# Kernel optimization log

Hardware: AMD Instinct MI355X
Metric: run time of the kernel (lower is better)

The kernel has to match this reference:

```python
import jax, jax.numpy as jnp
import numpy as np

N = 100000
E = 1600000
IN_DIM = 64
EMB_DIM = 64
BN_EPS = 1e-5


def setup_inputs() -> dict:
    key = jax.random.key(0)
    ks = jax.random.split(key, 8)
    x = jax.random.normal(ks[0], (N, IN_DIM), dtype=jnp.float32)
    edge_index = jax.random.randint(ks[1], (2, E), 0, N, dtype=jnp.int64)
    # GIN learned epsilon (train_eps=True), initialized to 0 as in PyG
    eps = jnp.zeros((), dtype=jnp.float32)
    # MLP params: Linear(in, emb) -> BN -> ReLU -> Linear(emb, emb)
    s1 = 1.0 / np.sqrt(IN_DIM)
    W1 = jax.random.uniform(ks[2], (IN_DIM, EMB_DIM), jnp.float32, -s1, s1)
    b1 = jax.random.uniform(ks[3], (EMB_DIM,), jnp.float32, -s1, s1)
    gamma = jnp.ones((EMB_DIM,), jnp.float32)
    beta = jnp.zeros((EMB_DIM,), jnp.float32)
    s2 = 1.0 / np.sqrt(EMB_DIM)
    W2 = jax.random.uniform(ks[4], (EMB_DIM, EMB_DIM), jnp.float32, -s2, s2)
    b2 = jax.random.uniform(ks[5], (EMB_DIM,), jnp.float32, -s2, s2)
    return {"x": x, "edge_index": edge_index, "eps": eps,
            "W1": W1, "b1": b1, "gamma": gamma, "beta": beta,
            "W2": W2, "b2": b2}


def reference(x, edge_index, eps, W1, b1, gamma, beta, W2, b2):
    src, dst = edge_index[0], edge_index[1]
    # GIN aggregation: sum of neighbor (source) features at each destination
    agg = jax.ops.segment_sum(x[src], dst, num_segments=N)  # [N, IN_DIM]
    h = (1.0 + eps) * x + agg
    # MLP: Linear -> BatchNorm1d (training-mode batch stats) -> ReLU -> Linear
    h1 = h @ W1 + b1                                   # [N, EMB_DIM]
    mean = jnp.mean(h1, axis=0)
    var = jnp.mean((h1 - mean) ** 2, axis=0)           # biased var, as torch BN
    h1n = (h1 - mean) * jax.lax.rsqrt(var + BN_EPS) * gamma + beta
    h2 = jax.nn.relu(h1n)
    return h2 @ W2 + b2                                # [N, EMB_DIM]
```

## Files before the change

### kernel.cpp

```cpp
#include <hip/hip_runtime.h>

#define NNODES 100000
#define NEDGES 1600000
#define DIM 64
#define NB 782
#define NPB 256
#define CHUNK 6250
#define CAP 3968
#define HP 72
#define NTILES 6250
#define NSLICE 32

typedef __attribute__((ext_vector_type(4))) float f32x4;
typedef __attribute__((ext_vector_type(8))) short s16x8;

__device__ __forceinline__ unsigned short bf16_rne(float f) {
  unsigned u = __float_as_uint(f);
  u += 0x7FFF + ((u >> 16) & 1);
  return (unsigned short)(u >> 16);
}
__device__ __forceinline__ float bf16_to_f32(unsigned short h) {
  return __uint_as_float(((unsigned)h) << 16);
}

__global__ __launch_bounds__(1024) void prep_part_kernel(
    const float* __restrict__ x, unsigned short* __restrict__ xb,
    const int* __restrict__ ei, int* __restrict__ gcursor,
    int* __restrict__ bpart,
    const float* __restrict__ W1, const float* __restrict__ W2,
    unsigned short* __restrict__ Wp1, unsigned short* __restrict__ Wp2) {
  __shared__ int sd[1024];
  __shared__ int delta[1024];
  __shared__ int lcur[1024];
  __shared__ int wsum[16];
  __shared__ int stage[CHUNK];
  __shared__ unsigned short sbuck[CHUNK];
  int t = threadIdx.x;
  sd[t] = 0;
  for (int i = blockIdx.x * 1024 + t; i < NNODES * DIM / 4; i += NPB * 1024) {
    float4 v = ((const float4*)x)[i];
    ushort4 o;
    o.x = bf16_rne(v.x); o.y = bf16_rne(v.y);
    o.z = bf16_rne(v.z); o.w = bf16_rne(v.w);
    ((ushort4*)xb)[i] = o;
  }
  if (blockIdx.x == 0 && t < 128) {
    int lane = t & 63;
    const float* W = (t >= 64) ? W2 : W1;
    unsigned short* Wp = (t >= 64) ? Wp2 : Wp1;
    int q = lane >> 4, n16 = lane & 15;
#pragma unroll
    for (int f = 0; f < 8; ++f) {
      int kk = f >> 2, nt = f & 3;
#pragma unroll
      for (int j = 0; j < 8; ++j) {
        int k = kk * 32 + q * 8 + j;
        int n = nt * 16 + n16;
        Wp[f * 512 + lane * 8 + j] = bf16_rne(W[k * DIM + n]);
      }
    }
  }
  __syncthreads();
  int base = blockIdx.x * CHUNK;
  for (int i = t; i < CHUNK; i += 1024)
    atomicAdd(&sd[ei[NEDGES + base + i] >> 7], 1);
  __syncthreads();
  int v = sd[t];
  int lane = t & 63;
  int incl = v;
#pragma unroll
  for (int off = 1; off < 64; off <<= 1) {
    int n = __shfl_up(incl, off);
    if (lane >= off) incl += n;
  }
  if (lane == 63) wsum[t >> 6] = incl;
  __syncthreads();
  if (t < 16) {
    int w = wsum[t];
#pragma unroll
    for (int off = 1; off < 16; off <<= 1) {
      int n = __shfl_up(w, off);
      if (t >= off) w += n;
    }
    wsum[t] = w;
  }
  __syncthreads();
  int wid = t >> 6;
  if (wid) incl += wsum[wid - 1];
  int excl = incl - v;
  delta[t] = (v ? (t * CAP + atomicAdd(&gcursor[t], v)) : 0) - excl;
  lcur[t] = excl;
  __syncthreads();
  for (int i = t; i < CHUNK; i += 1024) {
    int s = ei[base + i];
    int d = ei[NEDGES + base + i];
    int b = d >> 7;
    int p = atomicAdd(&lcur[b], 1);
    stage[p] = ((d & 127) << 17) | s;
    sbuck[p] = (unsigned short)b;
  }
  __syncthreads();
  for (int i = t; i < CHUNK; i += 1024)
    bpart[delta[sbuck[i]] + i] = stage[i];
}

__global__ __launch_bounds__(512) void mega_kernel(
    const int* __restrict__ bpart, const int* __restrict__ gcursor,
    const unsigned short* __restrict__ xb, float* __restrict__ h1,
    const unsigned short* __restrict__ Wp, const float* __restrict__ b1,
    const float* __restrict__ epsp,
    float* __restrict__ sums32, float* __restrict__ sumsq32) {
  __shared__ int sd[128];
  __shared__ int cur[128];
  __shared__ int swv[2];
  __shared__ int stage[CAP];
  __shared__ __align__(16) unsigned short hbuf[128 * HP];
  __shared__ float lsum[DIM];
  __shared__ float lsq[DIM];
  int b = blockIdx.x;
  int t = threadIdx.x;
  if (t < 128) sd[t] = 0;
  if (t < DIM) { lsum[t] = 0.0f; lsq[t] = 0.0f; }
  __syncthreads();
  int pbase = b * CAP;
  int cnt = gcursor[b];
  for (int i = t; i < cnt; i += 512)
    atomicAdd(&sd[bpart[pbase + i] >> 17], 1);
  __syncthreads();
  int deg = 0, incl = 0;
  if (t < 128) {
    deg = sd[t];
    incl = deg;
#pragma unroll
    for (int off = 1; off < 64; off <<= 1) {
      int n = __shfl_up(incl, off);
      if ((t & 63) >= off) incl += n;
    }
    if ((t & 63) == 63) swv[t >> 6] = incl;
  }
  __syncthreads();
  if (t < 128) {
    if (t >= 64) incl += swv[0];
    sd[t] = incl;
    cur[t] = incl - deg;
  }
  __syncthreads();
  for (int i = t; i < cnt; i += 512) {
    int v = bpart[pbase + i];
    int p = atomicAdd(&cur[v >> 17], 1);
    stage[p] = v & 0x1FFFF;
  }
  __syncthreads();
  {
    int part = t & 7;
    int half = (t >> 3) & 1;
    int ng = t >> 4;
#pragma unroll 1
    for (int pass = 0; pass < 4; ++pass) {
      int nl = ng + pass * 32;
      int e0 = (nl == 0) ? 0 : sd[nl - 1];
      int e1 = sd[nl];
      f32x4 aA0 = {0.f,0.f,0.f,0.f}, aA1 = aA0, aB0 = aA0, aB1 = aA0;
      int e = e0;
      for (; e + 8 <= e1; e += 8) {
        int s0 = stage[e + 0 + half];
        int s1 = stage[e + 2 + half];
        int s2 = stage[e + 4 + half];
        int s3 = stage[e + 6 + half];
        s16x8 u0 = *(const s16x8*)(xb + (size_t)s0 * DIM + part * 8);
        s16x8 u1 = *(const s16x8*)(xb + (size_t)s1 * DIM + part * 8);
        s16x8 u2 = *(const s16x8*)(xb + (size_t)s2 * DIM + part * 8);
        s16x8 u3 = *(const s16x8*)(xb + (size_t)s3 * DIM + part * 8);
#pragma unroll
        for (int j = 0; j < 4; ++j) {
          aA0[j] += bf16_to_f32((unsigned short)u0[j]) +
                    bf16_to_f32((unsigned short)u2[j]);
          aA1[j] += bf16_to_f32((unsigned short)u0[j + 4]) +
                    bf16_to_f32((unsigned short)u2[j + 4]);
          aB0[j] += bf16_to_f32((unsigned short)u1[j]) +
                    bf16_to_f32((unsigned short)u3[j]);
          aB1[j] += bf16_to_f32((unsigned short)u1[j + 4]) +
                    bf16_to_f32((unsigned short)u3[j + 4]);
        }
      }
      for (; e + 2 <= e1; e += 2) {
        int s = stage[e + half];
        s16x8 u = *(const s16x8*)(xb + (size_t)s * DIM + part * 8);
#pragma unroll
        for (int j = 0; j < 4; ++j) {
          aA0[j] += bf16_to_f32((unsigned short)u[j]);
          aA1[j] += bf16_to_f32((unsigned short)u[j + 4]);
        }
      }
      if (e < e1 && half == 0) {
        int s = stage[e];
        s16x8 u = *(const s16x8*)(xb + (size_t)s * DIM + part * 8);
#pragma unroll
        for (int j = 0; j < 4; ++j) {
          aA0[j] += bf16_to_f32((unsigned short)u[j]);
          aA1[j] += bf16_to_f32((unsigned short)u[j + 4]);
        }
      }
      float r[8];
#pragma unroll
      for (int j = 0; j < 4; ++j) {
        r[j] = aA0[j] + aB0[j];
        r[j + 4] = aA1[j] + aB1[j];
      }
      s16x8 o;
#pragma unroll
      for (int j = 0; j < 8; ++j)
        o[j] = (short)bf16_rne(r[j] + __shfl_down(r[j], 8));
      if (half == 0)
        *(s16x8*)&hbuf[nl * HP + part * 8] = o;
    }
  }
  __syncthreads();
  {
    int wave = t >> 6;
    int lane = t & 63;
    int tile = b * 8 + wave;
    if (tile < NTILES) {
      int q = lane >> 4;
      int r16 = lane & 15;
      float onep = 1.0f + epsp[0];
      s16x8 bf[8];
#pragma unroll
      for (int f = 0; f < 8; ++f)
        bf[f] = ((const s16x8*)Wp)[f * 64 + lane];
      int lrow = wave * 16 + r16;
      int grow = b * 128 + lrow;
      const s16x8* xrow = (const s16x8*)(xb + (size_t)grow * DIM);
      f32x4 acc[4] = {{0.f,0.f,0.f,0.f},{0.f,0.f,0.f,0.f},
                      {0.f,0.f,0.f,0.f},{0.f,0.f,0.f,0.f}};
#pragma unroll
      for (int kk = 0; kk < 2; ++kk) {
        s16x8 xv = xrow[kk * 4 + q];
        s16x8 hv = *(const s16x8*)&hbuf[lrow * HP + kk * 32 + q * 8];
        s16x8 a;
#pragma unroll
        for (int j = 0; j < 8; ++j)
          a[j] = (short)bf16_rne(fmaf(onep,
                     bf16_to_f32((unsigned short)xv[j]),
                     bf16_to_f32((unsigned short)hv[j])));
#pragma unroll
        for (int nt = 0; nt < 4; ++nt)
          acc[nt] = __builtin_amdgcn_mfma_f32_16x16x32_bf16(
              a, bf[kk * 4 + nt], acc[nt], 0, 0, 0);
      }
      int orow = tile * 16 + q * 4;
#pragma unroll
      for (int nt = 0; nt < 4; ++nt) {
        int col = nt * 16 + r16;
        float bb = b1[col];
        float sl = 0.0f, ql = 0.0f;
#pragma unroll
        for (int r = 0; r < 4; ++r) {
          float v = acc[nt][r] + bb;
          h1[(size_t)(orow + r) * DIM + col] = v;
          sl += v;
          ql = fmaf(v, v, ql);
        }
        sl += __shfl_down(sl, 32); ql += __shfl_down(ql, 32);
        sl += __shfl_down(sl, 16); ql += __shfl_down(ql, 16);
        if (q == 0) {
          atomicAdd(&lsum[col], sl);
          atomicAdd(&lsq[col], ql);
        }
      }
    }
  }
  __syncthreads();
  if (t < DIM) {
    int sl = (b & (NSLICE - 1)) * DIM;
    atomicAdd(&sums32[sl + t], lsum[t]);
    atomicAdd(&sumsq32[sl + t], lsq[t]);
  }
}

__global__ __launch_bounds__(256) void fused2_kernel(
    const float* __restrict__ h1, float* __restrict__ out,
    const unsigned short* __restrict__ Wp, const float* __restrict__ b2,
    const float* __restrict__ gamma, const float* __restrict__ beta,
    const float* __restrict__ sums32, const float* __restrict__ sumsq32) {
  __shared__ float sc_s[DIM];
  __shared__ float sh_s[DIM];
  int t = threadIdx.x;
  if (t < DIM) {
    float s = 0.0f, q2 = 0.0f;
#pragma unroll
    for (int j = 0; j < NSLICE; ++j) {
      s  += sums32[j * DIM + t];
      q2 += sumsq32[j * DIM + t];
    }
    float invN = 1.0f / (float)NNODES;
    float m = s * invN;
    float v = fmaf(-m, m, q2 * invN);
    float sc = gamma[t] * rsqrtf(v + 1e-5f);
    sc_s[t] = sc;
    sh_s[t] = fmaf(-m, sc, beta[t]);
  }
  __syncthreads();
  int wave = t >> 6;
  int lane = t & 63;
  int tile = blockIdx.x * 4 + wave;
  if (tile >= NTILES) return;
  int q = lane >> 4;
  int r16 = lane & 15;
  s16x8 bf[8];
#pragma unroll
  for (int f = 0; f < 8; ++f)
    bf[f] = ((const s16x8*)Wp)[f * 64 + lane];
  int arow = tile * 16 + r16;
  const float* hr = h1 + (size_t)arow * DIM + q * 8;
  f32x4 acc[4] = {{0.f,0.f,0.f,0.f},{0.f,0.f,0.f,0.f},
                  {0.f,0.f,0.f,0.f},{0.f,0.f,0.f,0.f}};
#pragma unroll
  for (int kk = 0; kk < 2; ++kk) {
    int kbase = kk * 32 + q * 8;
    float4 hv0 = *(const float4*)(hr + kk * 32);
    float4 hv1 = *(const float4*)(hr + kk * 32 + 4);
    float4 sc0 = *(const float4*)(sc_s + kbase);
    float4 sc1 = *(const float4*)(sc_s + kbase + 4);
    float4 sh0 = *(const float4*)(sh_s + kbase);
    float4 sh1 = *(const float4*)(sh_s + kbase + 4);
    s16x8 a;
    a[0] = (short)bf16_rne(fmaxf(fmaf(hv0.x, sc0.x, sh0.x), 0.f));
    a[1] = (short)bf16_rne(fmaxf(fmaf(hv0.y, sc0.y, sh0.y), 0.f));
    a[2] = (short)bf16_rne(fmaxf(fmaf(hv0.z, sc0.z, sh0.z), 0.f));
    a[3] = (short)bf16_rne(fmaxf(fmaf(hv0.w, sc0.w, sh0.w), 0.f));
    a[4] = (short)bf16_rne(fmaxf(fmaf(hv1.x, sc1.x, sh1.x), 0.f));
    a[5] = (short)bf16_rne(fmaxf(fmaf(hv1.y, sc1.y, sh1.y), 0.f));
    a[6] = (short)bf16_rne(fmaxf(fmaf(hv1.z, sc1.z, sh1.z), 0.f));
    a[7] = (short)bf16_rne(fmaxf(fmaf(hv1.w, sc1.w, sh1.w), 0.f));
#pragma unroll
    for (int nt = 0; nt < 4; ++nt)
      acc[nt] = __builtin_amdgcn_mfma_f32_16x16x32_bf16(
          a, bf[kk * 4 + nt], acc[nt], 0, 0, 0);
  }
  int orow = tile * 16 + q * 4;
#pragma unroll
  for (int nt = 0; nt < 4; ++nt) {
    int col = nt * 16 + r16;
    float bb = b2[col];
#pragma unroll
    for (int r = 0; r < 4; ++r)
      out[(size_t)(orow + r) * DIM + col] = acc[nt][r] + bb;
  }
}

extern "C" void kernel_launch(void* const* d_in, const int* in_sizes, int n_in,
                              void* d_out, int out_size, void* d_ws, size_t ws_size,
                              hipStream_t stream) {
  (void)in_sizes; (void)n_in; (void)out_size; (void)ws_size;
  const float* x     = (const float*)d_in[0];
  const int*   ei    = (const int*)d_in[1];
  const float* eps   = (const float*)d_in[2];
  const float* W1    = (const float*)d_in[3];
  const float* b1    = (const float*)d_in[4];
  const float* gamma = (const float*)d_in[5];
  const float* beta  = (const float*)d_in[6];
  const float* W2    = (const float*)d_in[7];
  const float* b2    = (const float*)d_in[8];
  float* outp = (float*)d_out;

  const int N = NNODES;

  float* h1       = (float*)d_ws;
  float* sums32   = h1 + (size_t)N * DIM;
  float* sumsq32  = sums32 + NSLICE * DIM;
  int*   gcursor  = (int*)(sumsq32 + NSLICE * DIM);
  unsigned short* Wp1 = (unsigned short*)(gcursor + 1024);
  unsigned short* Wp2 = Wp1 + 4096;
  int*            bpart = (int*)d_out;
  unsigned short* xb    = (unsigned short*)d_out + (size_t)NB * CAP * 2;

  hipMemsetAsync(sums32, 0,
                 (size_t)(2 * NSLICE * DIM) * sizeof(float) + 1024 * sizeof(int),
                 stream);
  prep_part_kernel<<<NPB, 1024, 0, stream>>>(x, xb, ei, gcursor, bpart,
                                             W1, W2, Wp1, Wp2);
  mega_kernel     <<<NB, 512, 0, stream>>>(bpart, gcursor, xb, h1,
                                           Wp1, b1, eps, sums32, sumsq32);
  fused2_kernel   <<<(NTILES + 3) / 4, 256, 0, stream>>>(h1, outp, Wp2, b2,
                                                         gamma, beta,
                                                         sums32, sumsq32);
}
```

Before: 159.4 us.

## Fuse second MLP stage into mega kernel via grid-wide barrier, drop h1 buffer

The BatchNorm/ReLU/second-GEMM stage is merged into the aggregation kernel. The first GEMM's accumulators stay in registers across a software grid barrier, an atomic counter with sleep-polling that waits for all blocks' BN statistics. Normalized activations are staged in LDS as bf16 for the second MFMA GEMM, which removes the global h1 write and read and one kernel launch. The partition kernel also doubles its block count and halves its chunk size. The grid barrier depends on all 782 blocks being co-resident, and it deadlocks if occupancy is ever insufficient.

```diff
diff --git a/kernel.cpp b/kernel.cpp
--- a/kernel.cpp
+++ b/kernel.cpp
@@ -4,8 +4,8 @@
 #define NEDGES 1600000
 #define DIM 64
 #define NB 782
-#define NPB 256
-#define CHUNK 6250
+#define NPB 512
+#define CHUNK 3125
 #define CAP 3968
 #define HP 72
 #define NTILES 6250
@@ -34,7 +34,7 @@
   __shared__ int lcur[1024];
   __shared__ int wsum[16];
   __shared__ int stage[CHUNK];
-  __shared__ unsigned short sbuck[CHUNK];
+  __shared__ unsigned short sbuck[CHUNK + 1];
   int t = threadIdx.x;
   sd[t] = 0;
   for (int i = blockIdx.x * 1024 + t; i < NNODES * DIM / 4; i += NPB * 1024) {
@@ -104,15 +104,18 @@
     bpart[delta[sbuck[i]] + i] = stage[i];
 }
 
-__global__ __launch_bounds__(512) void mega_kernel(
+__global__ __launch_bounds__(512, 8) void mega_kernel(
     const int* __restrict__ bpart, const int* __restrict__ gcursor,
-    const unsigned short* __restrict__ xb, float* __restrict__ h1,
-    const unsigned short* __restrict__ Wp, const float* __restrict__ b1,
+    const unsigned short* __restrict__ xb, float* __restrict__ out,
+    const unsigned short* __restrict__ Wp, const unsigned short* __restrict__ Wp2,
+    const float* __restrict__ b1, const float* __restrict__ b2,
+    const float* __restrict__ gamma, const float* __restrict__ beta,
     const float* __restrict__ epsp,
-    float* __restrict__ sums32, float* __restrict__ sumsq32) {
+    float* __restrict__ sums32, float* __restrict__ sumsq32,
+    int* __restrict__ gbar) {
   __shared__ int sd[128];
   __shared__ int cur[128];
-  __shared__ int swv[2];
+  __shared__ int swv[4];
   __shared__ int stage[CAP];
   __shared__ __align__(16) unsigned short hbuf[128 * HP];
   __shared__ float lsum[DIM];
@@ -216,57 +219,52 @@
     }
   }
   __syncthreads();
-  {
-    int wave = t >> 6;
-    int lane = t & 63;
-    int tile = b * 8 + wave;
-    if (tile < NTILES) {
-      int q = lane >> 4;
-      int r16 = lane & 15;
-      float onep = 1.0f + epsp[0];
-      s16x8 bf[8];
-#pragma unroll
-      for (int f = 0; f < 8; ++f)
-        bf[f] = ((const s16x8*)Wp)[f * 64 + lane];
-      int lrow = wave * 16 + r16;
-      int grow = b * 128 + lrow;
-      const s16x8* xrow = (const s16x8*)(xb + (size_t)grow * DIM);
-      f32x4 acc[4] = {{0.f,0.f,0.f,0.f},{0.f,0.f,0.f,0.f},
-                      {0.f,0.f,0.f,0.f},{0.f,0.f,0.f,0.f}};
-#pragma unroll
-      for (int kk = 0; kk < 2; ++kk) {
-        s16x8 xv = xrow[kk * 4 + q];
-        s16x8 hv = *(const s16x8*)&hbuf[lrow * HP + kk * 32 + q * 8];
-        s16x8 a;
-#pragma unroll
-        for (int j = 0; j < 8; ++j)
-          a[j] = (short)bf16_rne(fmaf(onep,
-                     bf16_to_f32((unsigned short)xv[j]),
-                     bf16_to_f32((unsigned short)hv[j])));
-#pragma unroll
-        for (int nt = 0; nt < 4; ++nt)
-          acc[nt] = __builtin_amdgcn_mfma_f32_16x16x32_bf16(
-              a, bf[kk * 4 + nt], acc[nt], 0, 0, 0);
-      }
-      int orow = tile * 16 + q * 4;
+  int wave = t >> 6;
+  int lane = t & 63;
+  int tile = b * 8 + wave;
+  int q = lane >> 4;
+  int r16 = lane & 15;
+  f32x4 acc[4] = {{0.f,0.f,0.f,0.f},{0.f,0.f,0.f,0.f},
+                  {0.f,0.f,0.f,0.f},{0.f,0.f,0.f,0.f}};
+  if (tile < NTILES) {
+    float onep = 1.0f + epsp[0];
+    int lrow = wave * 16 + r16;
+    int grow = b * 128 + lrow;
+    const s16x8* xrow = (const s16x8*)(xb + (size_t)grow * DIM);
+#pragma unroll
+    for (int kk = 0; kk < 2; ++kk) {
+      s16x8 xv = xrow[kk * 4 + q];
+      s16x8 hv = *(const s16x8*)&hbuf[lrow * HP + kk * 32 + q * 8];
+      s16x8 a;
+#pragma unroll
+      for (int j = 0; j < 8; ++j)
+        a[j] = (short)bf16_rne(fmaf(onep,
+                   bf16_to_f32((unsigned short)xv[j]),
+                   bf16_to_f32((unsigned short)hv[j])));
 #pragma unroll
       for (int nt = 0; nt < 4; ++nt) {
-        int col = nt * 16 + r16;
-        float bb = b1[col];
-        float sl = 0.0f, ql = 0.0f;
-#pragma unroll
-        for (int r = 0; r < 4; ++r) {
-          float v = acc[nt][r] + bb;
-          h1[(size_t)(orow + r) * DIM + col] = v;
-          sl += v;
-          ql = fmaf(v, v, ql);
-        }
-        sl += __shfl_down(sl, 32); ql += __shfl_down(ql, 32);
-        sl += __shfl_down(sl, 16); ql += __shfl_down(ql, 16);
-        if (q == 0) {
-          atomicAdd(&lsum[col], sl);
-          atomicAdd(&lsq[col], ql);
-        }
+        s16x8 bfk = ((const s16x8*)Wp)[(kk * 4 + nt) * 64 + lane];
+        acc[nt] = __builtin_amdgcn_mfma_f32_16x16x32_bf16(
+            a, bfk, acc[nt], 0, 0, 0);
+      }
+    }
+#pragma unroll
+    for (int nt = 0; nt < 4; ++nt) {
+      int col = nt * 16 + r16;
+      float bb = b1[col];
+      float sl = 0.0f, ql = 0.0f;
+#pragma unroll
+      for (int r = 0; r < 4; ++r) {
+        acc[nt][r] += bb;
+        float v = acc[nt][r];
+        sl += v;
+        ql = fmaf(v, v, ql);
+      }
+      sl += __shfl_down(sl, 32); ql += __shfl_down(ql, 32);
+      sl += __shfl_down(sl, 16); ql += __shfl_down(ql, 16);
+      if (q == 0) {
+        atomicAdd(&lsum[col], sl);
+        atomicAdd(&lsq[col], ql);
       }
     }
   }
@@ -276,76 +274,69 @@
     atomicAdd(&sums32[sl + t], lsum[t]);
     atomicAdd(&sumsq32[sl + t], lsq[t]);
   }
-}
-
-__global__ __launch_bounds__(256) void fused2_kernel(
-    const float* __restrict__ h1, float* __restrict__ out,
-    const unsigned short* __restrict__ Wp, const float* __restrict__ b2,
-    const float* __restrict__ gamma, const float* __restrict__ beta,
-    const float* __restrict__ sums32, const float* __restrict__ sumsq32) {
-  __shared__ float sc_s[DIM];
-  __shared__ float sh_s[DIM];
-  int t = threadIdx.x;
+  __syncthreads();
+  if (t == 0) {
+    __threadfence();
+    atomicAdd(gbar, 1);
+    while (__hip_atomic_load(gbar, __ATOMIC_ACQUIRE,
+                             __HIP_MEMORY_SCOPE_AGENT) < NB)
+      __builtin_amdgcn_s_sleep(8);
+  }
+  __syncthreads();
   if (t < DIM) {
     float s = 0.0f, q2 = 0.0f;
 #pragma unroll
     for (int j = 0; j < NSLICE; ++j) {
-      s  += sums32[j * DIM + t];
-      q2 += sumsq32[j * DIM + t];
+      s  += __hip_atomic_load(&sums32[j * DIM + t], __ATOMIC_RELAXED,
+                              __HIP_MEMORY_SCOPE_AGENT);
+      q2 += __hip_atomic_load(&sumsq32[j * DIM + t], __ATOMIC_RELAXED,
+                              __HIP_MEMORY_SCOPE_AGENT);
     }
     float invN = 1.0f / (float)NNODES;
     float m = s * invN;
     float v = fmaf(-m, m, q2 * invN);
     float sc = gamma[t] * rsqrtf(v + 1e-5f);
-    sc_s[t] = sc;
-    sh_s[t] = fmaf(-m, sc, beta[t]);
-  }
-  __syncthreads();
-  int wave = t >> 6;
-  int lane = t & 63;
-  int tile = blockIdx.x * 4 + wave;
-  if (tile >= NTILES) return;
-  int q = lane >> 4;
-  int r16 = lane & 15;
-  s16x8 bf[8];
-#pragma unroll
-  for (int f = 0; f < 8; ++f)
-    bf[f] = ((const s16x8*)Wp)[f * 64 + lane];
-  int arow = tile * 16 + r16;
-  const float* hr = h1 + (size_t)arow * DIM + q * 8;
-  f32x4 acc[4] = {{0.f,0.f,0.f,0.f},{0.f,0.f,0.f,0.f},
-                  {0.f,0.f,0.f,0.f},{0.f,0.f,0.f,0.f}};
-#pragma unroll
-  for (int kk = 0; kk < 2; ++kk) {
-    int kbase = kk * 32 + q * 8;
-    float4 hv0 = *(const float4*)(hr + kk * 32);
-    float4 hv1 = *(const float4*)(hr + kk * 32 + 4);
-    float4 sc0 = *(const float4*)(sc_s + kbase);
-    float4 sc1 = *(const float4*)(sc_s + kbase + 4);
-    float4 sh0 = *(const float4*)(sh_s + kbase);
-    float4 sh1 = *(const float4*)(sh_s + kbase + 4);
-    s16x8 a;
-    a[0] = (short)bf16_rne(fmaxf(fmaf(hv0.x, sc0.x, sh0.x), 0.f));
-    a[1] = (short)bf16_rne(fmaxf(fmaf(hv0.y, sc0.y, sh0.y), 0.f));
-    a[2] = (short)bf16_rne(fmaxf(fmaf(hv0.z, sc0.z, sh0.z), 0.f));
-    a[3] = (short)bf16_rne(fmaxf(fmaf(hv0.w, sc0.w, sh0.w), 0.f));
-    a[4] = (short)bf16_rne(fmaxf(fmaf(hv1.x, sc1.x, sh1.x), 0.f));
-    a[5] = (short)bf16_rne(fmaxf(fmaf(hv1.y, sc1.y, sh1.y), 0.f));
-    a[6] = (short)bf16_rne(fmaxf(fmaf(hv1.z, sc1.z, sh1.z), 0.f));
-    a[7] = (short)bf16_rne(fmaxf(fmaf(hv1.w, sc1.w, sh1.w), 0.f));
-#pragma unroll
-    for (int nt = 0; nt < 4; ++nt)
-      acc[nt] = __builtin_amdgcn_mfma_f32_16x16x32_bf16(
-          a, bf[kk * 4 + nt], acc[nt], 0, 0, 0);
-  }
-  int orow = tile * 16 + q * 4;
-#pragma unroll
-  for (int nt = 0; nt < 4; ++nt) {
-    int col = nt * 16 + r16;
-    float bb = b2[col];
-#pragma unroll
-    for (int r = 0; r < 4; ++r)
-      out[(size_t)(orow + r) * DIM + col] = acc[nt][r] + bb;
+    lsum[t] = sc;
+    lsq[t]  = fmaf(-m, sc, beta[t]);
+  }
+  __syncthreads();
+  if (tile < NTILES) {
+#pragma unroll
+    for (int nt = 0; nt < 4; ++nt) {
+      int col = nt * 16 + r16;
+      float sc = lsum[col];
+      float sh = lsq[col];
+#pragma unroll
+      for (int r = 0; r < 4; ++r) {
+        float y = fmaxf(fmaf(acc[nt][r], sc, sh), 0.0f);
+        hbuf[(wave * 16 + q * 4 + r) * HP + col] = bf16_rne(y);
+      }
+    }
+  }
+  __syncthreads();
+  if (tile < NTILES) {
+    int lrow = wave * 16 + r16;
+    f32x4 acc2[4] = {{0.f,0.f,0.f,0.f},{0.f,0.f,0.f,0.f},
+                     {0.f,0.f,0.f,0.f},{0.f,0.f,0.f,0.f}};
+#pragma unroll
+    for (int kk = 0; kk < 2; ++kk) {
+      s16x8 hv = *(const s16x8*)&hbuf[lrow * HP + kk * 32 + q * 8];
+#pragma unroll
+      for (int nt = 0; nt < 4; ++nt) {
+        s16x8 bfk = ((const s16x8*)Wp2)[(kk * 4 + nt) * 64 + lane];
+        acc2[nt] = __builtin_amdgcn_mfma_f32_16x16x32_bf16(
+            hv, bfk, acc2[nt], 0, 0, 0);
+      }
+    }
+    int orow = tile * 16 + q * 4;
+#pragma unroll
+    for (int nt = 0; nt < 4; ++nt) {
+      int col = nt * 16 + r16;
+      float bb = b2[col];
+#pragma unroll
+      for (int r = 0; r < 4; ++r)
+        out[(size_t)(orow + r) * DIM + col] = acc2[nt][r] + bb;
+    }
   }
 }
 
@@ -364,25 +355,22 @@
   const float* b2    = (const float*)d_in[8];
   float* outp = (float*)d_out;
 
-  const int N = NNODES;
-
-  float* h1       = (float*)d_ws;
-  float* sums32   = h1 + (size_t)N * DIM;
+  float* sums32   = (float*)d_ws;
   float* sumsq32  = sums32 + NSLICE * DIM;
   int*   gcursor  = (int*)(sumsq32 + NSLICE * DIM);
-  unsigned short* Wp1 = (unsigned short*)(gcursor + 1024);
+  int*   gbar     = gcursor + 1024;
+  unsigned short* Wp1 = (unsigned short*)(gbar + 4);
   unsigned short* Wp2 = Wp1 + 4096;
   int*            bpart = (int*)d_out;
   unsigned short* xb    = (unsigned short*)d_out + (size_t)NB * CAP * 2;
 
   hipMemsetAsync(sums32, 0,
-                 (size_t)(2 * NSLICE * DIM) * sizeof(float) + 1024 * sizeof(int),
+                 (size_t)(2 * NSLICE * DIM) * sizeof(float) +
+                     1024 * sizeof(int) + 4 * sizeof(int),
                  stream);
   prep_part_kernel<<<NPB, 1024, 0, stream>>>(x, xb, ei, gcursor, bpart,
                                              W1, W2, Wp1, Wp2);
-  mega_kernel     <<<NB, 512, 0, stream>>>(bpart, gcursor, xb, h1,
-                                           Wp1, b1, eps, sums32, sumsq32);
-  fused2_kernel   <<<(NTILES + 3) / 4, 256, 0, stream>>>(h1, outp, Wp2, b2,
-                                                         gamma, beta,
-                                                         sums32, sumsq32);
-}
+  mega_kernel     <<<NB, 512, 0, stream>>>(bpart, gcursor, xb, outp,
+                                           Wp1, Wp2, b1, b2, gamma, beta,
+                                           eps, sums32, sumsq32, gbar);
+}
```

New measurement: 309.6 us. 1.94x slower.

## Double partition blocks, register-cache edge loads, and load weights per MFMA

Applied to the files above, without the earlier changes.

The prep/partition kernel now launches twice as many blocks, each with half the edge chunk. Edge src/dst values are loaded once into registers and reused for both the histogram and scatter passes instead of being reread from global memory. The mega kernel likewise holds its bucketed edge words in registers across the count and placement passes, and loads weight fragments just before each MFMA rather than all up front. This cuts redundant global reads and may lower register pressure, but more blocks means more gcursor atomics and smaller per-block buckets.

```diff
diff --git a/kernel.cpp b/kernel.cpp
--- a/kernel.cpp
+++ b/kernel.cpp
@@ -4,8 +4,8 @@
 #define NEDGES 1600000
 #define DIM 64
 #define NB 782
-#define NPB 256
-#define CHUNK 6250
+#define NPB 512
+#define CHUNK 3125
 #define CAP 3968
 #define HP 72
 #define NTILES 6250
@@ -34,7 +34,7 @@
   __shared__ int lcur[1024];
   __shared__ int wsum[16];
   __shared__ int stage[CHUNK];
-  __shared__ unsigned short sbuck[CHUNK];
+  __shared__ unsigned short sbuck[CHUNK + 1];
   int t = threadIdx.x;
   sd[t] = 0;
   for (int i = blockIdx.x * 1024 + t; i < NNODES * DIM / 4; i += NPB * 1024) {
@@ -62,8 +62,15 @@
   }
   __syncthreads();
   int base = blockIdx.x * CHUNK;
-  for (int i = t; i < CHUNK; i += 1024)
-    atomicAdd(&sd[ei[NEDGES + base + i] >> 7], 1);
+  int es[4], ed[4];
+#pragma unroll
+  for (int j = 0; j < 4; ++j) {
+    int i = t + j * 1024;
+    bool ok = (i < CHUNK);
+    es[j] = ok ? ei[base + i] : 0;
+    ed[j] = ok ? ei[NEDGES + base + i] : -1;
+    if (ok) atomicAdd(&sd[ed[j] >> 7], 1);
+  }
   __syncthreads();
   int v = sd[t];
   int lane = t & 63;
@@ -91,13 +98,15 @@
   delta[t] = (v ? (t * CAP + atomicAdd(&gcursor[t], v)) : 0) - excl;
   lcur[t] = excl;
   __syncthreads();
-  for (int i = t; i < CHUNK; i += 1024) {
-    int s = ei[base + i];
-    int d = ei[NEDGES + base + i];
-    int b = d >> 7;
-    int p = atomicAdd(&lcur[b], 1);
-    stage[p] = ((d & 127) << 17) | s;
-    sbuck[p] = (unsigned short)b;
+#pragma unroll
+  for (int j = 0; j < 4; ++j) {
+    int i = t + j * 1024;
+    if (i < CHUNK) {
+      int b = ed[j] >> 7;
+      int p = atomicAdd(&lcur[b], 1);
+      stage[p] = ((ed[j] & 127) << 17) | es[j];
+      sbuck[p] = (unsigned short)b;
+    }
   }
   __syncthreads();
   for (int i = t; i < CHUNK; i += 1024)
@@ -112,7 +121,7 @@
     float* __restrict__ sums32, float* __restrict__ sumsq32) {
   __shared__ int sd[128];
   __shared__ int cur[128];
-  __shared__ int swv[2];
+  __shared__ int swv[4];
   __shared__ int stage[CAP];
   __shared__ __align__(16) unsigned short hbuf[128 * HP];
   __shared__ float lsum[DIM];
@@ -124,8 +133,13 @@
   __syncthreads();
   int pbase = b * CAP;
   int cnt = gcursor[b];
-  for (int i = t; i < cnt; i += 512)
-    atomicAdd(&sd[bpart[pbase + i] >> 17], 1);
+  int mv[8];
+#pragma unroll
+  for (int j = 0; j < 8; ++j) {
+    int i = t + j * 512;
+    mv[j] = (i < cnt) ? bpart[pbase + i] : -1;
+    if (mv[j] >= 0) atomicAdd(&sd[mv[j] >> 17], 1);
+  }
   __syncthreads();
   int deg = 0, incl = 0;
   if (t < 128) {
@@ -145,10 +159,12 @@
     cur[t] = incl - deg;
   }
   __syncthreads();
-  for (int i = t; i < cnt; i += 512) {
-    int v = bpart[pbase + i];
-    int p = atomicAdd(&cur[v >> 17], 1);
-    stage[p] = v & 0x1FFFF;
+#pragma unroll
+  for (int j = 0; j < 8; ++j) {
+    if (mv[j] >= 0) {
+      int p = atomicAdd(&cur[mv[j] >> 17], 1);
+      stage[p] = mv[j] & 0x1FFFF;
+    }
   }
   __syncthreads();
   {
@@ -224,10 +240,6 @@
       int q = lane >> 4;
       int r16 = lane & 15;
       float onep = 1.0f + epsp[0];
-      s16x8 bf[8];
-#pragma unroll
-      for (int f = 0; f < 8; ++f)
-        bf[f] = ((const s16x8*)Wp)[f * 64 + lane];
       int lrow = wave * 16 + r16;
       int grow = b * 128 + lrow;
       const s16x8* xrow = (const s16x8*)(xb + (size_t)grow * DIM);
@@ -244,9 +256,11 @@
                      bf16_to_f32((unsigned short)xv[j]),
                      bf16_to_f32((unsigned short)hv[j])));
 #pragma unroll
-        for (int nt = 0; nt < 4; ++nt)
+        for (int nt = 0; nt < 4; ++nt) {
+          s16x8 bfk = ((const s16x8*)Wp)[(kk * 4 + nt) * 64 + lane];
           acc[nt] = __builtin_amdgcn_mfma_f32_16x16x32_bf16(
-              a, bf[kk * 4 + nt], acc[nt], 0, 0, 0);
+              a, bfk, acc[nt], 0, 0, 0);
+        }
       }
       int orow = tile * 16 + q * 4;
 #pragma unroll
```

New measurement: 162.3 us. No clear change (+1.8%).
